# Kernel optimization log

Measured on AMD Instinct MI355X. Metric: run time of the kernel, lower is better.

The kernel has to match this reference:

```python
import jax, jax.numpy as jnp
import numpy as np
from jax import lax

B, C, H, W = 64, 3, 224, 224
P, NP, D, HEADS, DEPTH = 16, 196, 384, 6, 6
DD, DHEADS, DDEPTH = 256, 8, 4
NVIS = 49


def setup_inputs():
    key = jax.random.key(0)
    ks = iter(jax.random.split(key, 64))
    def rn(shape, s=0.02):
        return jax.random.normal(next(ks), shape, jnp.float32) * s
    perms = jax.vmap(lambda k: jax.random.permutation(k, NP))(jax.random.split(next(ks), B))
    inp = {
        'x': jax.random.normal(next(ks), (B, C, H, W), jnp.float32),
        'unmasked_idx': perms[:, :NVIS].astype(jnp.int32),
        'masked_idx': perms[:, NVIS:].astype(jnp.int32),
        'conv_w': rn((D, C, P, P)), 'conv_b': jnp.zeros((D,), jnp.float32),
        'cls_token': rn((D,)), 'pos_embed': rn((NP + 1, D)),
        'enc_ln1_w': jnp.ones((DEPTH, D), jnp.float32), 'enc_ln1_b': jnp.zeros((DEPTH, D), jnp.float32),
        'enc_qkv_w': rn((DEPTH, 3 * D, D)), 'enc_qkv_b': jnp.zeros((DEPTH, 3 * D), jnp.float32),
        'enc_out_w': rn((DEPTH, D, D)), 'enc_out_b': jnp.zeros((DEPTH, D), jnp.float32),
        'enc_ln2_w': jnp.ones((DEPTH, D), jnp.float32), 'enc_ln2_b': jnp.zeros((DEPTH, D), jnp.float32),
        'enc_fc1_w': rn((DEPTH, 4 * D, D)), 'enc_fc1_b': jnp.zeros((DEPTH, 4 * D), jnp.float32),
        'enc_fc2_w': rn((DEPTH, D, 4 * D)), 'enc_fc2_b': jnp.zeros((DEPTH, D), jnp.float32),
        'enc_norm_w': jnp.ones((D,), jnp.float32), 'enc_norm_b': jnp.zeros((D,), jnp.float32),
        'dec_embed_w': rn((DD, D)), 'dec_embed_b': jnp.zeros((DD,), jnp.float32),
        'mask_token': rn((DD,)), 'dec_pos_embed': rn((NP + 1, DD)),
        'dec_ln1_w': jnp.ones((DDEPTH, DD), jnp.float32), 'dec_ln1_b': jnp.zeros((DDEPTH, DD), jnp.float32),
        'dec_qkv_w': rn((DDEPTH, 3 * DD, DD)), 'dec_qkv_b': jnp.zeros((DDEPTH, 3 * DD), jnp.float32),
        'dec_out_w': rn((DDEPTH, DD, DD)), 'dec_out_b': jnp.zeros((DDEPTH, DD), jnp.float32),
        'dec_ln2_w': jnp.ones((DDEPTH, DD), jnp.float32), 'dec_ln2_b': jnp.zeros((DDEPTH, DD), jnp.float32),
        'dec_fc1_w': rn((DDEPTH, 4 * DD, DD)), 'dec_fc1_b': jnp.zeros((DDEPTH, 4 * DD), jnp.float32),
        'dec_fc2_w': rn((DDEPTH, DD, 4 * DD)), 'dec_fc2_b': jnp.zeros((DDEPTH, DD), jnp.float32),
        'dec_norm_w': jnp.ones((DD,), jnp.float32), 'dec_norm_b': jnp.zeros((DD,), jnp.float32),
        'pred_w': rn((P * P * 3, DD)), 'pred_b': jnp.zeros((P * P * 3,), jnp.float32),
    }
    return inp


def layer_norm(x, w, b, eps=1e-5):
    m = x.mean(-1, keepdims=True)
    v = ((x - m) ** 2).mean(-1, keepdims=True)
    return (x - m) * lax.rsqrt(v + eps) * w + b


def mha(x, wqkv, bqkv, wo, bo, h):
    b, s, d = x.shape
    dh = d // h
    qkv = x @ wqkv.T + bqkv
    q, k, v = jnp.split(qkv, 3, axis=-1)
    sp = lambda t: t.reshape(b, s, h, dh).transpose(0, 2, 1, 3)  # [b,h,s,dh]
    q, k, v = sp(q), sp(k), sp(v)
    scores = jnp.einsum('bhqd,bhkd->bhqk', q, k) * (1.0 / np.sqrt(dh))
    a = jax.nn.softmax(scores, axis=-1)
    o = jnp.einsum('bhqk,bhkd->bhqd', a, v).transpose(0, 2, 1, 3).reshape(b, s, d)
    return o @ wo.T + bo


def run_blocks(x, depth, heads, ln1_w, ln1_b, qkv_w, qkv_b, out_w, out_b, ln2_w, ln2_b, fc1_w, fc1_b, fc2_w, fc2_b):
    for i in range(depth):
        x = x + mha(layer_norm(x, ln1_w[i], ln1_b[i]), qkv_w[i], qkv_b[i], out_w[i], out_b[i], heads)
        hdn = jax.nn.gelu(layer_norm(x, ln2_w[i], ln2_b[i]) @ fc1_w[i].T + fc1_b[i], approximate=False)
        x = x + hdn @ fc2_w[i].T + fc2_b[i]
    return x


def reference(x, unmasked_idx, masked_idx, conv_w, conv_b, cls_token, pos_embed,
              enc_ln1_w, enc_ln1_b, enc_qkv_w, enc_qkv_b, enc_out_w, enc_out_b,
              enc_ln2_w, enc_ln2_b, enc_fc1_w, enc_fc1_b, enc_fc2_w, enc_fc2_b,
              enc_norm_w, enc_norm_b, dec_embed_w, dec_embed_b, mask_token, dec_pos_embed,
              dec_ln1_w, dec_ln1_b, dec_qkv_w, dec_qkv_b, dec_out_w, dec_out_b,
              dec_ln2_w, dec_ln2_b, dec_fc1_w, dec_fc1_b, dec_fc2_w, dec_fc2_b,
              dec_norm_w, dec_norm_b, pred_w, pred_b):
    b = x.shape[0]
    # patch embed: conv stride=kernel=16 -> [B, D, 14, 14] -> [B, 196, D]
    p = lax.conv_general_dilated(x, conv_w, (P, P), 'VALID',
                                 dimension_numbers=('NCHW', 'OIHW', 'NCHW'))
    p = p.reshape(b, D, NP).transpose(0, 2, 1) + conv_b + pos_embed[1:]
    bi = jnp.arange(b)[:, None]
    vis = p[bi, unmasked_idx]                      # [B, NVIS, D] per-sample gather
    cls = cls_token + pos_embed[0]
    xe = jnp.concatenate([jnp.broadcast_to(cls, (b, 1, D)), vis], axis=1)
    xe = run_blocks(xe, DEPTH, HEADS, enc_ln1_w, enc_ln1_b, enc_qkv_w, enc_qkv_b,
                    enc_out_w, enc_out_b, enc_ln2_w, enc_ln2_b, enc_fc1_w, enc_fc1_b,
                    enc_fc2_w, enc_fc2_b)
    xe = layer_norm(xe, enc_norm_w, enc_norm_b)
    xd = xe @ dec_embed_w.T + dec_embed_b          # [B, 1+NVIS, DD]
    vis_dec = xd[:, 1:, :]                         # drop cls
    full = jnp.zeros((b, NP, DD), xd.dtype)
    full = full.at[bi, unmasked_idx].set(vis_dec)  # scatter visible tokens
    full = full.at[bi, masked_idx].set(mask_token) # scatter mask tokens
    full = full + dec_pos_embed[1:]
    xf = run_blocks(full, DDEPTH, DHEADS, dec_ln1_w, dec_ln1_b, dec_qkv_w, dec_qkv_b,
                    dec_out_w, dec_out_b, dec_ln2_w, dec_ln2_b, dec_fc1_w, dec_fc1_b,
                    dec_fc2_w, dec_fc2_b)
    xf = layer_norm(xf, dec_norm_w, dec_norm_b)
    return xf @ pred_w.T + pred_b                  # [B, NP, P*P*3]
```

## Files before the change

### kernel.cpp

```cpp
#include <hip/hip_runtime.h>
#include <hip/hip_bf16.h>

#define B_    64
#define NP_   196
#define NVIS_ 49
#define D_    384
#define DD_   256
#define SENC_ 50
#define SDEC_ 196

typedef __hip_bfloat16 bf16;
typedef __attribute__((ext_vector_type(8))) short short8;
typedef __attribute__((ext_vector_type(4))) float float4v;

__device__ __forceinline__ float bf2f(bf16 x) { return __bfloat162float(x); }
__device__ __forceinline__ bf16 f2bf(float x) { return __float2bfloat16(x); }
__device__ __forceinline__ float rdin(const void* p, long i, int f) {
  return f ? ((const float*)p)[i] : bf2f(((const bf16*)p)[i]);
}

__global__ void probe_kernel(const void* w, int* flag) {
  int tid = threadIdx.x;
  float mx = 0.f;
  for (int i = tid; i < 512; i += 64)
    mx = fmaxf(mx, fabsf(bf2f(((const bf16*)w)[i])));
#pragma unroll
  for (int off = 32; off; off >>= 1) mx = fmaxf(mx, __shfl_xor(mx, off));
  if (tid == 0) *flag = (mx > 1e3f) ? 1 : 0;
}

__global__ __launch_bounds__(256) void fill_kernel(bf16* out, float v, int n) {
  int idx = blockIdx.x * 256 + threadIdx.x;
  if (idx < n) out[idx] = f2bf(v);
}

__global__ __launch_bounds__(256) void im2col_vis_kernel(
    const void* __restrict__ x, const int* __restrict__ unmasked,
    bf16* __restrict__ out, const int* __restrict__ dflag) {
  int f = *dflag;
  int idx = blockIdx.x * 256 + threadIdx.x;
  const int TOT = B_ * NVIS_ * 768;
  if (idx >= TOT) return;
  int k = idx % 768;
  int row = idx / 768;
  int j = row % NVIS_;
  int b = row / NVIS_;
  int n = unmasked[b * NVIS_ + j];
  int ph = n / 14, pw = n % 14;
  int c  = k >> 8;
  int rr = (k >> 4) & 15;
  int cc = k & 15;
  out[idx] = f2bf(rdin(x, (long)(((b * 3 + c) * 224) + ph * 16 + rr) * 224 + pw * 16 + cc, f));
}

#define LDK 40
template <int MODE, int TMW, int TNW>
__global__ __launch_bounds__(256) void gemm_kernel(
    const bf16* __restrict__ A, const void* __restrict__ W, long wOff,
    const void* __restrict__ bias, long bOff,
    void* __restrict__ C, int M, int N, int K, int KS, int out_mode,
    const int* __restrict__ dflag) {
  constexpr int BM = 2 * TMW, BN = 2 * TNW;
  constexpr int AM = TMW / 16, AN = TNW / 16;
  int f = *dflag;
  __shared__ bf16 Asl[BM * LDK];
  __shared__ bf16 Bsl[BN * LDK];
  int tid = threadIdx.x;
  int bx = blockIdx.x, by = blockIdx.y, bz = blockIdx.z;
  int w = tid >> 6, lane = tid & 63;
  int quad = lane >> 4, l16 = lane & 15;
  int wm = (w & 1) * TMW, wn = (w >> 1) * TNW;
  int tr = tid >> 2, tc = (tid & 3) * 8;
  const bf16* Ab = A + (long)by * BM * K;
  long wBase = wOff + (long)bx * BN * K;
  int k0lo = bz * KS;

  float4v acc[AM][AN];
#pragma unroll
  for (int i = 0; i < AM; i++)
#pragma unroll
    for (int j = 0; j < AN; j++) acc[i][j] = (float4v){0.f, 0.f, 0.f, 0.f};

  for (int k0 = k0lo; k0 < k0lo + KS; k0 += 32) {
#pragma unroll
    for (int h2 = 0; h2 < BM / 64; h2++) {
      int r = tr + h2 * 64;
      uint4 v = *(const uint4*)(Ab + (long)r * K + k0 + tc);
      *(uint4*)(&Asl[r * LDK + tc]) = v;
    }
    if (f) {
#pragma unroll
      for (int h2 = 0; h2 < BN / 64; h2++) {
        int r = tr + h2 * 64;
        const float* p = (const float*)W + wBase + (long)r * K + k0 + tc;
        float4 v0 = *(const float4*)p;
        float4 v1 = *(const float4*)(p + 4);
        union { uint4 u; bf16 hh[8]; } pk;
        pk.hh[0] = f2bf(v0.x); pk.hh[1] = f2bf(v0.y);
        pk.hh[2] = f2bf(v0.z); pk.hh[3] = f2bf(v0.w);
        pk.hh[4] = f2bf(v1.x); pk.hh[5] = f2bf(v1.y);
        pk.hh[6] = f2bf(v1.z); pk.hh[7] = f2bf(v1.w);
        *(uint4*)(&Bsl[r * LDK + tc]) = pk.u;
      }
    } else {
#pragma unroll
      for (int h2 = 0; h2 < BN / 64; h2++) {
        int r = tr + h2 * 64;
        uint4 v = *(const uint4*)((const bf16*)W + wBase + (long)r * K + k0 + tc);
        *(uint4*)(&Bsl[r * LDK + tc]) = v;
      }
    }
    __syncthreads();
    short8 af[AM], bfr[AN];
#pragma unroll
    for (int mi = 0; mi < AM; mi++)
      af[mi] = *(const short8*)&Asl[(wm + mi * 16 + l16) * LDK + quad * 8];
#pragma unroll
    for (int ni = 0; ni < AN; ni++)
      bfr[ni] = *(const short8*)&Bsl[(wn + ni * 16 + l16) * LDK + quad * 8];
#pragma unroll
    for (int mi = 0; mi < AM; mi++)
#pragma unroll
      for (int ni = 0; ni < AN; ni++)
        acc[mi][ni] = __builtin_amdgcn_mfma_f32_16x16x32_bf16(
            af[mi], bfr[ni], acc[mi][ni], 0, 0, 0);
    __syncthreads();
  }

  int om = (out_mode == 2) ? (f ? 1 : 0) : out_mode;
  float* Cf = (float*)C + (long)bz * M * N;
  bf16*  Cb = (bf16*)C;
#pragma unroll
  for (int mi = 0; mi < AM; mi++) {
#pragma unroll
    for (int ni = 0; ni < AN; ni++) {
      int cn = bx * BN + wn + ni * 16 + l16;
      float bval = (bz == 0) ? rdin(bias, bOff + cn, f) : 0.f;
#pragma unroll
      for (int r = 0; r < 4; r++) {
        int cm = by * BM + wm + mi * 16 + quad * 4 + r;
        float v = acc[mi][ni][r] + bval;
        if constexpr (MODE == 1) v = 0.5f * v * (1.0f + erff(v * 0.70710678f));
        if (om) Cf[(long)cm * N + cn] = v;
        else    Cb[(long)cm * N + cn] = f2bf(v);
      }
    }
  }
}

template <int N>
__global__ __launch_bounds__(256) void ln_kernel(
    float* __restrict__ X, const float* __restrict__ G0,
    const float* __restrict__ G1, const float* __restrict__ G2,
    const void* __restrict__ w, long wOff, const void* __restrict__ bv,
    long bOff, bf16* __restrict__ Y, int M, const int* __restrict__ dflag) {
  int f = *dflag;
  int row = blockIdx.x * 4 + (threadIdx.x >> 6);
  int lane = threadIdx.x & 63;
  if (row >= M) return;
  float* xr = X + (long)row * N;
  const float* g0 = G0 ? G0 + (long)row * N : nullptr;
  const float* g1 = G1 ? G1 + (long)row * N : nullptr;
  const float* g2 = G2 ? G2 + (long)row * N : nullptr;
  constexpr int CNT = N / 64;
  float v[CNT];
  float sum = 0.f;
#pragma unroll
  for (int i = 0; i < CNT; i++) {
    int c = lane + 64 * i;
    float t = xr[c];
    if (g0) t += g0[c];
    if (g1) t += g1[c];
    if (g2) t += g2[c];
    if (g0) xr[c] = t;
    v[i] = t;
    sum += t;
  }
#pragma unroll
  for (int off = 32; off; off >>= 1) sum += __shfl_xor(sum, off);
  float mean = sum * (1.0f / N);
  float vs = 0.f;
#pragma unroll
  for (int i = 0; i < CNT; i++) { float d = v[i] - mean; vs += d * d; }
#pragma unroll
  for (int off = 32; off; off >>= 1) vs += __shfl_xor(vs, off);
  float rstd = rsqrtf(vs * (1.0f / N) + 1e-5f);
  bf16* yr = Y + (long)row * N;
#pragma unroll
  for (int i = 0; i < CNT; i++) {
    int cidx = lane + 64 * i;
    yr[cidx] = f2bf((v[i] - mean) * rstd * rdin(w, wOff + cidx, f) + rdin(bv, bOff + cidx, f));
  }
}

__global__ __launch_bounds__(256) void attn_dec_kernel(
    const bf16* __restrict__ qkv, bf16* __restrict__ out) {
  const int S = SDEC_, DH = 32, Dm = 256, tri = 768;
  const int KLD = 40, VLD = 232, PLD = 232;
  int b = blockIdx.x >> 3, h = blockIdx.x & 7;
  __shared__ bf16 Ksh[208 * KLD];
  __shared__ bf16 Vt[32 * VLD];
  __shared__ bf16 Psh[4][16 * PLD];
  int tid = threadIdx.x;
  const bf16* base = qkv + (long)b * S * tri;
  for (int idx = tid; idx < S * 4; idx += 256) {
    int s = idx >> 2, part = (idx & 3) * 8;
    uint4 v = *(const uint4*)(base + (long)s * tri + Dm + h * DH + part);
    *(uint4*)(&Ksh[s * KLD + part]) = v;
  }
  if (tid < 12 * 4) {
    int s = 196 + (tid >> 2), part = (tid & 3) * 8;
    uint4 z = {0, 0, 0, 0};
    *(uint4*)(&Ksh[s * KLD + part]) = z;
  }
  for (int idx = tid; idx < S * DH; idx += 256) {
    int s = idx >> 5, d = idx & 31;
    Vt[d * VLD + s] = base[(long)s * tri + 2 * Dm + h * DH + d];
  }
  for (int idx = tid; idx < 32 * 36; idx += 256) {
    int d = idx / 36, c = 196 + idx % 36;
    Vt[d * VLD + c] = f2bf(0.f);
  }
  __syncthreads();
  int w = tid >> 6, lane = tid & 63, l16 = lane & 15, quad = lane >> 4;
  bf16* Pw = &Psh[w][0];
  const float scale = 0.17677669529663687f;
  for (int qt = w; qt < 13; qt += 4) {
    int q0 = qt * 16;
    int qr = min(q0 + l16, S - 1);
    short8 qf = *(const short8*)(base + (long)qr * tri + h * DH + quad * 8);
    float4v sc[13];
#pragma unroll
    for (int t = 0; t < 13; t++) {
      short8 kf = *(const short8*)&Ksh[(t * 16 + l16) * KLD + quad * 8];
      sc[t] = __builtin_amdgcn_mfma_f32_16x16x32_bf16(
          qf, kf, (float4v){0.f, 0.f, 0.f, 0.f}, 0, 0, 0);
    }
    float mx[4] = {-1e30f, -1e30f, -1e30f, -1e30f};
#pragma unroll
    for (int t = 0; t < 13; t++) {
      bool valid = (t * 16 + l16) < S;
#pragma unroll
      for (int r = 0; r < 4; r++) {
        float v = valid ? sc[t][r] * scale : -1e30f;
        sc[t][r] = v;
        mx[r] = fmaxf(mx[r], v);
      }
    }
#pragma unroll
    for (int off = 1; off < 16; off <<= 1)
#pragma unroll
      for (int r = 0; r < 4; r++) mx[r] = fmaxf(mx[r], __shfl_xor(mx[r], off));
    float sm[4] = {0.f, 0.f, 0.f, 0.f};
#pragma unroll
    for (int t = 0; t < 13; t++)
#pragma unroll
      for (int r = 0; r < 4; r++) {
        float p = __expf(sc[t][r] - mx[r]);
        sc[t][r] = p;
        sm[r] += p;
      }
#pragma unroll
    for (int off = 1; off < 16; off <<= 1)
#pragma unroll
      for (int r = 0; r < 4; r++) sm[r] += __shfl_xor(sm[r], off);
#pragma unroll
    for (int t = 0; t < 14; t++) {
      int col = t * 16 + l16;
#pragma unroll
      for (int r = 0; r < 4; r++) {
        float p = (t < 13) ? sc[t][r] : 0.f;
        Pw[(quad * 4 + r) * PLD + col] = f2bf(p);
      }
    }
    __asm__ volatile("s_waitcnt lgkmcnt(0)" ::: "memory");
    float4v o0 = {0.f, 0.f, 0.f, 0.f}, o1 = {0.f, 0.f, 0.f, 0.f};
#pragma unroll
    for (int kc = 0; kc < 7; kc++) {
      short8 pf = *(const short8*)&Pw[l16 * PLD + kc * 32 + quad * 8];
      short8 v0 = *(const short8*)&Vt[l16 * VLD + kc * 32 + quad * 8];
      short8 v1 = *(const short8*)&Vt[(16 + l16) * VLD + kc * 32 + quad * 8];
      o0 = __builtin_amdgcn_mfma_f32_16x16x32_bf16(pf, v0, o0, 0, 0, 0);
      o1 = __builtin_amdgcn_mfma_f32_16x16x32_bf16(pf, v1, o1, 0, 0, 0);
    }
#pragma unroll
    for (int r = 0; r < 4; r++) {
      int row = q0 + quad * 4 + r;
      if (row < S) {
        float inv = 1.f / sm[r];
        bf16* op = out + ((long)(b * S + row)) * Dm + h * DH;
        op[l16]      = f2bf(o0[r] * inv);
        op[16 + l16] = f2bf(o1[r] * inv);
      }
    }
  }
}

__global__ __launch_bounds__(128) void attn_enc_kernel(
    const bf16* __restrict__ qkv, bf16* __restrict__ out) {
  const int S = SENC_, H = 6, DH = 64, Dm = H * DH, tri = 3 * Dm;
  int b = blockIdx.x / H, h = blockIdx.x % H;
  int tid = threadIdx.x;
  __shared__ float Ks[SENC_ * 64];
  __shared__ float Vs[SENC_ * 64];
  __shared__ float P1[SENC_ * 66];
  const bf16* base = qkv + (long)b * S * tri;
  for (int idx = tid; idx < S * 8; idx += 128) {
    int s = idx >> 3, part = (idx & 7) * 8;
    union { uint4 u; bf16 hh[8]; } kk, vv;
    kk.u = *(const uint4*)(base + (long)s * tri + Dm + h * DH + part);
    vv.u = *(const uint4*)(base + (long)s * tri + 2 * Dm + h * DH + part);
#pragma unroll
    for (int j = 0; j < 8; j++) {
      Ks[s * DH + part + j] = bf2f(kk.hh[j]);
      Vs[s * DH + part + j] = bf2f(vv.hh[j]);
    }
  }
  __syncthreads();
  int w = tid >> 6, lane = tid & 63;
  int row = lane;
  float q[DH], o[DH];
  float m = -1e30f, l = 0.f;
  if (lane < S) {
    const float scale = 0.125f;
#pragma unroll
    for (int d = 0; d < DH; d++) {
      q[d] = bf2f(base[(long)row * tri + h * DH + d]) * scale;
      o[d] = 0.f;
    }
    int jlo = w * 25, jhi = jlo + 25;
    for (int j = jlo; j < jhi; j++) {
      float s = 0.f;
#pragma unroll
      for (int d = 0; d < DH; d++) s += q[d] * Ks[j * DH + d];
      float mn = fmaxf(m, s);
      float corr = __expf(m - mn);
      float p = __expf(s - mn);
      l = l * corr + p;
      m = mn;
#pragma unroll
      for (int d = 0; d < DH; d++) o[d] = o[d] * corr + p * Vs[j * DH + d];
    }
    if (w == 1) {
#pragma unroll
      for (int d = 0; d < DH; d++) P1[row * 66 + d] = o[d];
      P1[row * 66 + 64] = m;
      P1[row * 66 + 65] = l;
    }
  }
  __syncthreads();
  if (w == 0 && lane < S) {
    float m1 = P1[row * 66 + 64], l1 = P1[row * 66 + 65];
    float mg = fmaxf(m, m1);
    float e0 = __expf(m - mg), e1 = __expf(m1 - mg);
    float lg = l * e0 + l1 * e1;
    float inv = 1.f / lg;
    bf16* op = out + ((long)(b * S + row) * Dm + h * DH);
#pragma unroll
    for (int d = 0; d < DH; d++)
      op[d] = f2bf((o[d] * e0 + P1[row * 66 + d] * e1) * inv);
  }
}

__global__ __launch_bounds__(256) void build_xe_kernel(
    const float* __restrict__ G0, const float* __restrict__ G1,
    const float* __restrict__ G2, const void* __restrict__ cls,
    const void* __restrict__ pos, const int* __restrict__ unmasked,
    float* __restrict__ xe, const int* __restrict__ dflag) {
  int f = *dflag;
  int idx = blockIdx.x * 256 + threadIdx.x;
  const int TOT = B_ * SENC_ * D_;
  if (idx >= TOT) return;
  int d = idx % D_;
  int s = (idx / D_) % SENC_;
  int b = idx / (D_ * SENC_);
  float v;
  if (s == 0) {
    v = rdin(cls, d, f) + rdin(pos, d, f);
  } else {
    int j = s - 1;
    int n = unmasked[b * NVIS_ + j];
    long r = (long)(b * NVIS_ + j) * D_ + d;
    v = G0[r] + G1[r] + G2[r] + rdin(pos, (long)(1 + n) * D_ + d, f);
  }
  xe[idx] = v;
}

__global__ __launch_bounds__(256) void dec_init_kernel(
    const void* __restrict__ mask_token, const void* __restrict__ dpos,
    float* __restrict__ full, const int* __restrict__ dflag) {
  int f = *dflag;
  int idx = blockIdx.x * 256 + threadIdx.x;
  const int TOT = B_ * NP_ * DD_;
  if (idx >= TOT) return;
  int d = idx % DD_;
  int n = (idx / DD_) % NP_;
  full[idx] = rdin(mask_token, d, f) + rdin(dpos, (long)(1 + n) * DD_ + d, f);
}

__global__ __launch_bounds__(256) void dec_scatter_kernel(
    const float* __restrict__ Gx0, const float* __restrict__ Gx1,
    const int* __restrict__ unmasked, const void* __restrict__ dpos,
    float* __restrict__ full, const int* __restrict__ dflag) {
  int f = *dflag;
  int idx = blockIdx.x * 256 + threadIdx.x;
  const int TOT = B_ * NVIS_ * DD_;
  if (idx >= TOT) return;
  int d = idx % DD_;
  int j = (idx / DD_) % NVIS_;
  int b = idx / (DD_ * NVIS_);
  int n = unmasked[b * NVIS_ + j];
  long r = (long)(b * SENC_ + 1 + j) * DD_ + d;
  full[((long)(b * NP_ + n)) * DD_ + d] =
      Gx0[r] + Gx1[r] + rdin(dpos, (long)(1 + n) * DD_ + d, f);
}

extern "C" void kernel_launch(void* const* d_in, const int* in_sizes, int n_in,
                              void* d_out, int out_size, void* d_ws, size_t ws_size,
                              hipStream_t stream) {
  (void)in_sizes; (void)n_in;
  const int* unmasked = (const int*)d_in[1];
  const int M_ENC = B_ * SENC_;
  const int M_DEC = B_ * NP_;

  const size_t NEEDED = 58884100;
  if (ws_size < NEEDED) {
    fill_kernel<<<(out_size + 255) / 256, 256, 0, stream>>>(
        (bf16*)d_out, (float)(ws_size >> 20), out_size);
    return;
  }
  char* wsb = (char*)d_ws;
  bf16*  big    = (bf16*)wsb;
  float* full   = (float*)(wsb + 25690112);
  bf16*  im2col = (bf16*)(wsb + 25690112);
  bf16*  t0     = (bf16*)(wsb + 38535168);
  float* xe     = (float*)(wsb + 44957696);
  float* Gdec   = (float*)(wsb + 44957696);
  int*   dflag  = (int*)(wsb + 58884096);
  float* Gp0 = (float*)(wsb + 0);
  float* Gp1 = (float*)(wsb + 4915200);
  float* Gp2 = (float*)(wsb + 9830400);
  float* Gf0 = (float*)(wsb + 9830400);
  float* Gf1 = (float*)(wsb + 14745600);
  float* Gf2 = (float*)(wsb + 19660800);
  float* Gx0 = (float*)(wsb + 0);
  float* Gx1 = (float*)(wsb + 3276800);

  probe_kernel<<<1, 64, 0, stream>>>(d_in[3], dflag);

  auto gemm = [&](int mode, int cfg, const bf16* A, const void* W, long wOff,
                  const void* bias, long bOff, void* C,
                  int M, int N, int K, int splits, int out_mode) {
    int BM = (cfg == 2) ? 64 : 128;
    int BN = (cfg == 0) ? 128 : 64;
    dim3 g(N / BN, M / BM, splits);
    int KS = K / splits;
#define GL(MO, TM, TN) gemm_kernel<MO, TM, TN><<<g, 256, 0, stream>>>( \
        A, W, wOff, bias, bOff, C, M, N, K, KS, out_mode, dflag)
    if (mode == 0) {
      if (cfg == 0) GL(0, 64, 64); else if (cfg == 1) GL(0, 64, 32); else GL(0, 32, 32);
    } else {
      if (cfg == 0) GL(1, 64, 64); else if (cfg == 1) GL(1, 64, 32); else GL(1, 32, 32);
    }
#undef GL
  };

  {
    int tot = B_ * NVIS_ * 768;
    im2col_vis_kernel<<<(tot + 255) / 256, 256, 0, stream>>>(d_in[0], unmasked, im2col, dflag);
    gemm(0, 2, im2col, d_in[3], 0, d_in[4], 0, Gp0, 3200, D_, 768, 3, 1);
    int tot2 = B_ * SENC_ * D_;
    build_xe_kernel<<<(tot2 + 255) / 256, 256, 0, stream>>>(
        Gp0, Gp1, Gp2, d_in[5], d_in[6], unmasked, xe, dflag);
  }

  const float *eg0 = nullptr, *eg1 = nullptr, *eg2 = nullptr;
  for (int i = 0; i < 6; i++) {
    ln_kernel<D_><<<M_ENC / 4, 256, 0, stream>>>(
        xe, eg0, eg1, eg2, d_in[7], (long)i * D_, d_in[8], (long)i * D_, t0, M_ENC, dflag);
    gemm(0, 2, t0, d_in[9], (long)i * 3 * D_ * D_, d_in[10], (long)i * 3 * D_, big, M_ENC, 3 * D_, D_, 1, 0);
    attn_enc_kernel<<<B_ * 6, 128, 0, stream>>>(big, t0);
    gemm(0, 2, t0, d_in[11], (long)i * D_ * D_, d_in[12], (long)i * D_, Gp0, M_ENC, D_, D_, 2, 1);
    ln_kernel<D_><<<M_ENC / 4, 256, 0, stream>>>(
        xe, Gp0, Gp1, nullptr, d_in[13], (long)i * D_, d_in[14], (long)i * D_, t0, M_ENC, dflag);
    gemm(1, 2, t0, d_in[15], (long)i * 4 * D_ * D_, d_in[16], (long)i * 4 * D_, big, M_ENC, 4 * D_, D_, 1, 0);
    gemm(0, 2, big, d_in[17], (long)i * D_ * 4 * D_, d_in[18], (long)i * D_, Gf0, M_ENC, D_, 4 * D_, 3, 1);
    eg0 = Gf0; eg1 = Gf1; eg2 = Gf2;
  }
  ln_kernel<D_><<<M_ENC / 4, 256, 0, stream>>>(
      xe, Gf0, Gf1, Gf2, d_in[19], 0, d_in[20], 0, t0, M_ENC, dflag);
  gemm(0, 2, t0, d_in[21], 0, d_in[22], 0, Gx0, M_ENC, DD_, D_, 2, 1);

  {
    int tot = B_ * NP_ * DD_;
    dec_init_kernel<<<(tot + 255) / 256, 256, 0, stream>>>(d_in[23], d_in[24], full, dflag);
    int tot2 = B_ * NVIS_ * DD_;
    dec_scatter_kernel<<<(tot2 + 255) / 256, 256, 0, stream>>>(
        Gx0, Gx1, unmasked, d_in[24], full, dflag);
  }

  const float* dg = nullptr;
  for (int i = 0; i < 4; i++) {
    ln_kernel<DD_><<<M_DEC / 4, 256, 0, stream>>>(
        full, dg, nullptr, nullptr, d_in[25], (long)i * DD_, d_in[26], (long)i * DD_, t0, M_DEC, dflag);
    gemm(0, 1, t0, d_in[27], (long)i * 3 * DD_ * DD_, d_in[28], (long)i * 3 * DD_, big, M_DEC, 3 * DD_, DD_, 1, 0);
    attn_dec_kernel<<<B_ * 8, 256, 0, stream>>>(big, t0);
    gemm(0, 2, t0, d_in[29], (long)i * DD_ * DD_, d_in[30], (long)i * DD_, Gdec, M_DEC, DD_, DD_, 1, 1);
    ln_kernel<DD_><<<M_DEC / 4, 256, 0, stream>>>(
        full, Gdec, nullptr, nullptr, d_in[31], (long)i * DD_, d_in[32], (long)i * DD_, t0, M_DEC, dflag);
    gemm(1, 1, t0, d_in[33], (long)i * 4 * DD_ * DD_, d_in[34], (long)i * DD_ * 4, big, M_DEC, 4 * DD_, DD_, 1, 0);
    gemm(0, 2, big, d_in[35], (long)i * DD_ * 4 * DD_, d_in[36], (long)i * DD_, Gdec, M_DEC, DD_, 4 * DD_, 1, 1);
    dg = Gdec;
  }
  ln_kernel<DD_><<<M_DEC / 4, 256, 0, stream>>>(
      full, Gdec, nullptr, nullptr, d_in[37], 0, d_in[38], 0, t0, M_DEC, dflag);

  gemm(0, 1, t0, d_in[39], 0, d_in[40], 0, d_out, M_DEC, 768, DD_, 1, 2);
}
```

Baseline: 1.516 ms.

## Double-buffer GEMM LDS tiles with K=64 stages and XCD-aware block remap

```diff
diff --git a/kernel.cpp b/kernel.cpp
--- a/kernel.cpp
+++ b/kernel.cpp
@@ -53,7 +53,7 @@
   out[idx] = f2bf(rdin(x, (long)(((b * 3 + c) * 224) + ph * 16 + rr) * 224 + pw * 16 + cc, f));
 }
 
-#define LDK 40
+#define LDK2 72
 template <int MODE, int TMW, int TNW>
 __global__ __launch_bounds__(256) void gemm_kernel(
     const bf16* __restrict__ A, const void* __restrict__ W, long wOff,
@@ -62,15 +62,23 @@
     const int* __restrict__ dflag) {
   constexpr int BM = 2 * TMW, BN = 2 * TNW;
   constexpr int AM = TMW / 16, AN = TNW / 16;
+  constexpr int AR = BM / 32, BR = BN / 32;
   int f = *dflag;
-  __shared__ bf16 Asl[BM * LDK];
-  __shared__ bf16 Bsl[BN * LDK];
+  __shared__ bf16 Asl[2][BM * LDK2];
+  __shared__ bf16 Bsl[2][BN * LDK2];
   int tid = threadIdx.x;
-  int bx = blockIdx.x, by = blockIdx.y, bz = blockIdx.z;
+
+  int gx = gridDim.x;
+  int nwg = gx * gridDim.y;
+  int orig = blockIdx.y * gx + blockIdx.x;
+  int q = nwg >> 3, rr_ = nwg & 7, xcd = orig & 7, off = orig >> 3;
+  int wgid = (xcd < rr_ ? xcd * (q + 1) : rr_ * (q + 1) + (xcd - rr_) * q) + off;
+  int bx = wgid % gx, by = wgid / gx, bz = blockIdx.z;
+
   int w = tid >> 6, lane = tid & 63;
   int quad = lane >> 4, l16 = lane & 15;
   int wm = (w & 1) * TMW, wn = (w >> 1) * TNW;
-  int tr = tid >> 2, tc = (tid & 3) * 8;
+  int rstg = tid >> 3, cstg = (tid & 7) * 8;
   const bf16* Ab = A + (long)by * BM * K;
   long wBase = wOff + (long)bx * BN * K;
   int k0lo = bz * KS;
@@ -81,50 +89,88 @@
 #pragma unroll
     for (int j = 0; j < AN; j++) acc[i][j] = (float4v){0.f, 0.f, 0.f, 0.f};
 
-  for (int k0 = k0lo; k0 < k0lo + KS; k0 += 32) {
-#pragma unroll
-    for (int h2 = 0; h2 < BM / 64; h2++) {
-      int r = tr + h2 * 64;
-      uint4 v = *(const uint4*)(Ab + (long)r * K + k0 + tc);
-      *(uint4*)(&Asl[r * LDK + tc]) = v;
+  uint4 apre[AR];
+  uint4 bpre_lo[BR], bpre_hi[BR];
+
+  auto loadTiles = [&](int k0) {
+#pragma unroll
+    for (int i = 0; i < AR; i++) {
+      int r = rstg + i * 32;
+      apre[i] = *(const uint4*)(Ab + (long)r * K + k0 + cstg);
     }
     if (f) {
 #pragma unroll
-      for (int h2 = 0; h2 < BN / 64; h2++) {
-        int r = tr + h2 * 64;
-        const float* p = (const float*)W + wBase + (long)r * K + k0 + tc;
-        float4 v0 = *(const float4*)p;
-        float4 v1 = *(const float4*)(p + 4);
+      for (int i = 0; i < BR; i++) {
+        int r = rstg + i * 32;
+        const float* p = (const float*)W + wBase + (long)r * K + k0 + cstg;
+        bpre_lo[i] = *(const uint4*)p;
+        bpre_hi[i] = *(const uint4*)(p + 4);
+      }
+    } else {
+#pragma unroll
+      for (int i = 0; i < BR; i++) {
+        int r = rstg + i * 32;
+        bpre_lo[i] = *(const uint4*)((const bf16*)W + wBase + (long)r * K + k0 + cstg);
+      }
+    }
+  };
+
+  auto commitTiles = [&](int buf) {
+#pragma unroll
+    for (int i = 0; i < AR; i++) {
+      int r = rstg + i * 32;
+      *(uint4*)(&Asl[buf][r * LDK2 + cstg]) = apre[i];
+    }
+    if (f) {
+#pragma unroll
+      for (int i = 0; i < BR; i++) {
+        int r = rstg + i * 32;
+        union { uint4 u; float ff[4]; } lo, hi;
+        lo.u = bpre_lo[i]; hi.u = bpre_hi[i];
         union { uint4 u; bf16 hh[8]; } pk;
-        pk.hh[0] = f2bf(v0.x); pk.hh[1] = f2bf(v0.y);
-        pk.hh[2] = f2bf(v0.z); pk.hh[3] = f2bf(v0.w);
-        pk.hh[4] = f2bf(v1.x); pk.hh[5] = f2bf(v1.y);
-        pk.hh[6] = f2bf(v1.z); pk.hh[7] = f2bf(v1.w);
-        *(uint4*)(&Bsl[r * LDK + tc]) = pk.u;
+        pk.hh[0] = f2bf(lo.ff[0]); pk.hh[1] = f2bf(lo.ff[1]);
+        pk.hh[2] = f2bf(lo.ff[2]); pk.hh[3] = f2bf(lo.ff[3]);
+        pk.hh[4] = f2bf(hi.ff[0]); pk.hh[5] = f2bf(hi.ff[1]);
+        pk.hh[6] = f2bf(hi.ff[2]); pk.hh[7] = f2bf(hi.ff[3]);
+        *(uint4*)(&Bsl[buf][r * LDK2 + cstg]) = pk.u;
       }
     } else {
 #pragma unroll
-      for (int h2 = 0; h2 < BN / 64; h2++) {
-        int r = tr + h2 * 64;
-        uint4 v = *(const uint4*)((const bf16*)W + wBase + (long)r * K + k0 + tc);
-        *(uint4*)(&Bsl[r * LDK + tc]) = v;
-      }
-    }
-    __syncthreads();
-    short8 af[AM], bfr[AN];
-#pragma unroll
-    for (int mi = 0; mi < AM; mi++)
-      af[mi] = *(const short8*)&Asl[(wm + mi * 16 + l16) * LDK + quad * 8];
-#pragma unroll
-    for (int ni = 0; ni < AN; ni++)
-      bfr[ni] = *(const short8*)&Bsl[(wn + ni * 16 + l16) * LDK + quad * 8];
-#pragma unroll
-    for (int mi = 0; mi < AM; mi++)
+      for (int i = 0; i < BR; i++) {
+        int r = rstg + i * 32;
+        *(uint4*)(&Bsl[buf][r * LDK2 + cstg]) = bpre_lo[i];
+      }
+    }
+  };
+
+  loadTiles(k0lo);
+  commitTiles(0);
+  __syncthreads();
+
+  int nst = KS >> 6;
+  for (int s = 0; s < nst; s++) {
+    int cur = s & 1;
+    if (s + 1 < nst) loadTiles(k0lo + (s + 1) * 64);
+#pragma unroll
+    for (int kk = 0; kk < 2; kk++) {
+      short8 af[AM], bfr[AN];
+#pragma unroll
+      for (int mi = 0; mi < AM; mi++)
+        af[mi] = *(const short8*)&Asl[cur][(wm + mi * 16 + l16) * LDK2 + kk * 32 + quad * 8];
 #pragma unroll
       for (int ni = 0; ni < AN; ni++)
-        acc[mi][ni] = __builtin_amdgcn_mfma_f32_16x16x32_bf16(
-            af[mi], bfr[ni], acc[mi][ni], 0, 0, 0);
-    __syncthreads();
+        bfr[ni] = *(const short8*)&Bsl[cur][(wn + ni * 16 + l16) * LDK2 + kk * 32 + quad * 8];
+#pragma unroll
+      for (int mi = 0; mi < AM; mi++)
+#pragma unroll
+        for (int ni = 0; ni < AN; ni++)
+          acc[mi][ni] = __builtin_amdgcn_mfma_f32_16x16x32_bf16(
+              af[mi], bfr[ni], acc[mi][ni], 0, 0, 0);
+    }
+    if (s + 1 < nst) {
+      commitTiles(cur ^ 1);
+      __syncthreads();
+    }
   }
 
   int om = (out_mode == 2) ? (f ? 1 : 0) : out_mode;
```

Result: slower. 3.131 ms (+106.5%).

## Double-buffer GEMM shared tiles with K=64 stages and XCD-aware block remap

Applied to the files above, without the earlier changes.

```diff
diff --git a/kernel.cpp b/kernel.cpp
--- a/kernel.cpp
+++ b/kernel.cpp
@@ -53,7 +53,8 @@
   out[idx] = f2bf(rdin(x, (long)(((b * 3 + c) * 224) + ph * 16 + rr) * 224 + pw * 16 + cc, f));
 }
 
-#define LDK 40
+#define LDK2 72
+#define UNR _Pragma("unroll")
 template <int MODE, int TMW, int TNW>
 __global__ __launch_bounds__(256) void gemm_kernel(
     const bf16* __restrict__ A, const void* __restrict__ W, long wOff,
@@ -62,17 +63,24 @@
     const int* __restrict__ dflag) {
   constexpr int BM = 2 * TMW, BN = 2 * TNW;
   constexpr int AM = TMW / 16, AN = TNW / 16;
+  constexpr int AR = BM / 32, BR = BN / 32;
   int f = *dflag;
-  __shared__ bf16 Asl[BM * LDK];
-  __shared__ bf16 Bsl[BN * LDK];
+  __shared__ bf16 Asl[2][BM * LDK2];
+  __shared__ bf16 Bsl[2][BN * LDK2];
   int tid = threadIdx.x;
-  int bx = blockIdx.x, by = blockIdx.y, bz = blockIdx.z;
+
+  int gx = gridDim.x;
+  int nwg = gx * gridDim.y;
+  int orig = blockIdx.y * gx + blockIdx.x;
+  int q = nwg >> 3, rr_ = nwg & 7, xcd = orig & 7, off = orig >> 3;
+  int wgid = (xcd < rr_ ? xcd * (q + 1) : rr_ * (q + 1) + (xcd - rr_) * q) + off;
+  int bx = wgid % gx, by = wgid / gx, bz = blockIdx.z;
+
   int w = tid >> 6, lane = tid & 63;
   int quad = lane >> 4, l16 = lane & 15;
   int wm = (w & 1) * TMW, wn = (w >> 1) * TNW;
-  int tr = tid >> 2, tc = (tid & 3) * 8;
-  const bf16* Ab = A + (long)by * BM * K;
-  long wBase = wOff + (long)bx * BN * K;
+  int rstg = tid >> 3, cstg = (tid & 7) * 8;
+  const bf16* Ab = A + (long)by * BM * K + (long)rstg * K + cstg;
   int k0lo = bz * KS;
 
   float4v acc[AM][AN];
@@ -81,51 +89,75 @@
 #pragma unroll
     for (int j = 0; j < AN; j++) acc[i][j] = (float4v){0.f, 0.f, 0.f, 0.f};
 
-  for (int k0 = k0lo; k0 < k0lo + KS; k0 += 32) {
-#pragma unroll
-    for (int h2 = 0; h2 < BM / 64; h2++) {
-      int r = tr + h2 * 64;
-      uint4 v = *(const uint4*)(Ab + (long)r * K + k0 + tc);
-      *(uint4*)(&Asl[r * LDK + tc]) = v;
-    }
-    if (f) {
-#pragma unroll
-      for (int h2 = 0; h2 < BN / 64; h2++) {
-        int r = tr + h2 * 64;
-        const float* p = (const float*)W + wBase + (long)r * K + k0 + tc;
-        float4 v0 = *(const float4*)p;
-        float4 v1 = *(const float4*)(p + 4);
-        union { uint4 u; bf16 hh[8]; } pk;
-        pk.hh[0] = f2bf(v0.x); pk.hh[1] = f2bf(v0.y);
-        pk.hh[2] = f2bf(v0.z); pk.hh[3] = f2bf(v0.w);
-        pk.hh[4] = f2bf(v1.x); pk.hh[5] = f2bf(v1.y);
-        pk.hh[6] = f2bf(v1.z); pk.hh[7] = f2bf(v1.w);
-        *(uint4*)(&Bsl[r * LDK + tc]) = pk.u;
-      }
-    } else {
-#pragma unroll
-      for (int h2 = 0; h2 < BN / 64; h2++) {
-        int r = tr + h2 * 64;
-        uint4 v = *(const uint4*)((const bf16*)W + wBase + (long)r * K + k0 + tc);
-        *(uint4*)(&Bsl[r * LDK + tc]) = v;
-      }
-    }
+#define LOAD_A(k0) UNR for (int i = 0; i < AR; i++) \
+    apre[i] = *(const uint4*)(Ab + (long)i * 32 * K + (k0));
+#define STORE_A(buf) UNR for (int i = 0; i < AR; i++) \
+    *(uint4*)(&Asl[buf][(rstg + i * 32) * LDK2 + cstg]) = apre[i];
+#define LOAD_BF(k0) UNR for (int i = 0; i < BR; i++) { \
+    const float* p_ = Wf + (long)i * 32 * K + (k0); \
+    blo[i] = *(const uint4*)p_; bhi[i] = *(const uint4*)(p_ + 4); }
+#define STORE_BF(buf) UNR for (int i = 0; i < BR; i++) { \
+    union { uint4 u; float ff[4]; } lo_, hi_; lo_.u = blo[i]; hi_.u = bhi[i]; \
+    union { uint4 u; bf16 hh[8]; } pk_; \
+    pk_.hh[0] = f2bf(lo_.ff[0]); pk_.hh[1] = f2bf(lo_.ff[1]); \
+    pk_.hh[2] = f2bf(lo_.ff[2]); pk_.hh[3] = f2bf(lo_.ff[3]); \
+    pk_.hh[4] = f2bf(hi_.ff[0]); pk_.hh[5] = f2bf(hi_.ff[1]); \
+    pk_.hh[6] = f2bf(hi_.ff[2]); pk_.hh[7] = f2bf(hi_.ff[3]); \
+    *(uint4*)(&Bsl[buf][(rstg + i * 32) * LDK2 + cstg]) = pk_.u; }
+#define LOAD_BH(k0) UNR for (int i = 0; i < BR; i++) \
+    blo[i] = *(const uint4*)(Wh + (long)i * 32 * K + (k0));
+#define STORE_BH(buf) UNR for (int i = 0; i < BR; i++) \
+    *(uint4*)(&Bsl[buf][(rstg + i * 32) * LDK2 + cstg]) = blo[i];
+#define COMPUTE(cur) UNR for (int kk = 0; kk < 2; kk++) { \
+    short8 af[AM], bfr[AN]; \
+    UNR for (int mi = 0; mi < AM; mi++) \
+      af[mi] = *(const short8*)&Asl[cur][(wm + mi * 16 + l16) * LDK2 + kk * 32 + quad * 8]; \
+    UNR for (int ni = 0; ni < AN; ni++) \
+      bfr[ni] = *(const short8*)&Bsl[cur][(wn + ni * 16 + l16) * LDK2 + kk * 32 + quad * 8]; \
+    UNR for (int mi = 0; mi < AM; mi++) \
+      UNR for (int ni = 0; ni < AN; ni++) \
+        acc[mi][ni] = __builtin_amdgcn_mfma_f32_16x16x32_bf16( \
+            af[mi], bfr[ni], acc[mi][ni], 0, 0, 0); }
+
+  int nst = KS >> 6;
+  if (f) {
+    const float* Wf = (const float*)W + wOff + (long)bx * BN * K + (long)rstg * K + cstg;
+    uint4 apre[AR], blo[BR], bhi[BR];
+    LOAD_A(k0lo); LOAD_BF(k0lo);
+    STORE_A(0);   STORE_BF(0);
     __syncthreads();
-    short8 af[AM], bfr[AN];
-#pragma unroll
-    for (int mi = 0; mi < AM; mi++)
-      af[mi] = *(const short8*)&Asl[(wm + mi * 16 + l16) * LDK + quad * 8];
-#pragma unroll
-    for (int ni = 0; ni < AN; ni++)
-      bfr[ni] = *(const short8*)&Bsl[(wn + ni * 16 + l16) * LDK + quad * 8];
-#pragma unroll
-    for (int mi = 0; mi < AM; mi++)
-#pragma unroll
-      for (int ni = 0; ni < AN; ni++)
-        acc[mi][ni] = __builtin_amdgcn_mfma_f32_16x16x32_bf16(
-            af[mi], bfr[ni], acc[mi][ni], 0, 0, 0);
+    for (int s = 0; s < nst - 1; s++) {
+      int cur = s & 1;
+      int k0 = k0lo + (s + 1) * 64;
+      LOAD_A(k0); LOAD_BF(k0);
+      COMPUTE(cur);
+      STORE_A(cur ^ 1); STORE_BF(cur ^ 1);
+      __syncthreads();
+    }
+    COMPUTE((nst - 1) & 1);
+  } else {
+    const bf16* Wh = (const bf16*)W + wOff + (long)bx * BN * K + (long)rstg * K + cstg;
+    uint4 apre[AR], blo[BR];
+    LOAD_A(k0lo); LOAD_BH(k0lo);
+    STORE_A(0);   STORE_BH(0);
     __syncthreads();
-  }
+    for (int s = 0; s < nst - 1; s++) {
+      int cur = s & 1;
+      int k0 = k0lo + (s + 1) * 64;
+      LOAD_A(k0); LOAD_BH(k0);
+      COMPUTE(cur);
+      STORE_A(cur ^ 1); STORE_BH(cur ^ 1);
+      __syncthreads();
+    }
+    COMPUTE((nst - 1) & 1);
+  }
+#undef LOAD_A
+#undef STORE_A
+#undef LOAD_BF
+#undef STORE_BF
+#undef LOAD_BH
+#undef STORE_BH
+#undef COMPUTE
 
   int om = (out_mode == 2) ? (f ? 1 : 0) : out_mode;
   float* Cf = (float*)C + (long)bz * M * N;
@@ -508,7 +540,7 @@
     gemm(0, 2, t0, d_in[29], (long)i * DD_ * DD_, d_in[30], (long)i * DD_, Gdec, M_DEC, DD_, DD_, 1, 1);
     ln_kernel<DD_><<<M_DEC / 4, 256, 0, stream>>>(
         full, Gdec, nullptr, nullptr, d_in[31], (long)i * DD_, d_in[32], (long)i * DD_, t0, M_DEC, dflag);
-    gemm(1, 1, t0, d_in[33], (long)i * 4 * DD_ * DD_, d_in[34], (long)i * DD_ * 4, big, M_DEC, 4 * DD_, DD_, 1, 0);
+    gemm(1, 0, t0, d_in[33], (long)i * 4 * DD_ * DD_, d_in[34], (long)i * DD_ * 4, big, M_DEC, 4 * DD_, DD_, 1, 0);
     gemm(0, 2, big, d_in[35], (long)i * DD_ * 4 * DD_, d_in[36], (long)i * DD_, Gdec, M_DEC, DD_, 4 * DD_, 1, 1);
     dg = Gdec;
   }
```

Result: faster. 1.369 ms (-9.7%).
